# Kernel tuning notes

Hardware: AMD Instinct MI355X
Metric: run time of the kernel (lower is better)

## Reference

```python
import jax, jax.numpy as jnp
import numpy as np

NCE_T = 0.07


def setup_inputs() -> dict:
    key = jax.random.key(0)
    k1, k2, k3 = jax.random.split(key, 3)
    features_1 = jax.random.normal(k1, (1, 20000, 256), dtype=jnp.float32)
    features_2 = jax.random.normal(k2, (1, 8192, 256), dtype=jnp.float32)
    map21 = jax.random.randint(k3, (8192,), 0, 20000, dtype=jnp.int64)
    return {"features_1": features_1, "features_2": features_2, "map21": map21}


def reference(features_1, features_2, map21):
    # squeeze leading batch dim (module assumes batch size 1)
    f1 = features_1[0]  # [N1, D]
    f2 = features_2[0]  # [P, D]  (P == nce_num_pairs == len(map21) -> arange branch)
    query = f1[map21]   # [P, D] gather
    keys = f2           # [P, D]
    # pairwise Euclidean distance via matmul trick (matches torch.cdist p=2)
    q_sq = jnp.sum(query * query, axis=-1)  # [P]
    k_sq = jnp.sum(keys * keys, axis=-1)    # [P]
    sq_dist = q_sq[:, None] + k_sq[None, :] - 2.0 * (query @ keys.T)  # [P, P]
    dist = jnp.sqrt(jnp.maximum(sq_dist, 0.0))
    logits = -dist / NCE_T
    # cross entropy with labels = arange(P): mean of -log_softmax diagonal
    logp = jax.nn.log_softmax(logits, axis=-1)
    loss = -jnp.mean(jnp.diagonal(logp))
    return loss
```

## Files before the change

### kernel.cpp

```cpp
#include <hip/hip_runtime.h>
#include <hip/hip_bf16.h>

#define PP       8192
#define DIM      256
#define GS16     4096
#define NCHUNK   16
#define TCOLS    32
#define ROWBLK   256
#define NROWBLK  (PP / ROWBLK)

typedef __bf16 bf16_t;
using bf16x8 = __attribute__((ext_vector_type(8))) __bf16;
using bf16x4 = __attribute__((ext_vector_type(4))) __bf16;
using f32x4  = __attribute__((ext_vector_type(4))) float;

#define C2    20.609929155556618
#define MEXP  (-340.0f)
#define COEF  ((float)(-C2 * 8388608.0))
#define KBIAS ((float)((127.0 + 340.0) * 8388608.0))
#define LN2   0.6931471805599453f


__global__ __launch_bounds__(256) void nce_prep(
    const float* __restrict__ f1, const float* __restrict__ f2,
    const int* __restrict__ map,
    bf16_t* __restrict__ qb2, bf16_t* __restrict__ kb2,
    float* __restrict__ qsq, float* __restrict__ ksq,
    float* __restrict__ diag2, float* __restrict__ part_l,
    unsigned* __restrict__ cnt, float* __restrict__ out)
{
    const int tid  = threadIdx.x;
    const int wave = tid >> 6, lane = tid & 63;
    const int p    = blockIdx.x * 4 + wave;
    const int gtid = blockIdx.x * 256 + tid;

    if (gtid < PP) part_l[gtid] = 0.0f;
    if (gtid < NROWBLK) cnt[gtid] = 0u;
    if (gtid == 0) out[0] = 0.0f;

    const int idx = map[p];
    const f32x4 qv = *(const f32x4*)(f1 + (size_t)idx * DIM + lane * 4);
    const f32x4 kv = *(const f32x4*)(f2 + (size_t)p * DIM + lane * 4);

    float qs = qv[0]*qv[0] + qv[1]*qv[1] + qv[2]*qv[2] + qv[3]*qv[3];
    float ks = kv[0]*kv[0] + kv[1]*kv[1] + kv[2]*kv[2] + kv[3]*kv[3];
    const f32x4 dv = qv - kv;
    float ds = dv[0]*dv[0] + dv[1]*dv[1] + dv[2]*dv[2] + dv[3]*dv[3];

    bf16x4 qo, ko;
    #pragma unroll
    for (int i = 0; i < 4; ++i) { qo[i] = (bf16_t)qv[i]; ko[i] = (bf16_t)kv[i]; }

    const int G = p >> 4, l15 = p & 15;
    const size_t off = (size_t)G * GS16 + (size_t)(lane >> 3) * 512
                     + (size_t)(l15 + 16 * ((lane >> 1) & 3)) * 8 + (lane & 1) * 4;
    *(bf16x4*)(qb2 + off) = qo;
    *(bf16x4*)(kb2 + off) = ko;

    #pragma unroll
    for (int s = 32; s > 0; s >>= 1) {
        qs += __shfl_xor(qs, s);
        ks += __shfl_xor(ks, s);
        ds += __shfl_xor(ds, s);
    }
    if (lane == 0) {
        qsq[p]   = qs;
        ksq[p]   = ks;
        diag2[p] = (float)(-C2) * __builtin_amdgcn_sqrtf(ds);
    }
}

__global__ __launch_bounds__(256, 2) void nce_main(
    const bf16_t* __restrict__ qb2, const bf16_t* __restrict__ kb2,
    const float* __restrict__ qsq, const float* __restrict__ ksq,
    const float* __restrict__ diag2, float* __restrict__ part_l,
    unsigned* __restrict__ cnt, float* __restrict__ out)
{
    const int tid  = threadIdx.x, wave = tid >> 6, lane = tid & 63;
    const int quad = lane >> 4, l15 = lane & 15;
    const int rb   = blockIdx.x;
    const int ch   = blockIdx.y;
    const int Gb   = rb * 16 + wave * 4;
    const int rbase = rb * ROWBLK + wave * 64;

    __shared__ int   s_last;
    __shared__ float red[4];

    bf16x8 a[4][8];
    {
        const bf16_t* ap = qb2 + (size_t)Gb * GS16 + lane * 8;
        #pragma unroll
        for (int rg = 0; rg < 4; ++rg)
            #pragma unroll
            for (int f = 0; f < 8; ++f)
                a[rg][f] = *(const bf16x8*)(ap + rg * GS16 + f * 512);
    }

    float qs[16];
    #pragma unroll
    for (int i = 0; i < 16; ++i)
        qs[i] = qsq[rbase + (i >> 2) * 16 + quad * 4 + (i & 3)];

    float l[16];
    #pragma unroll
    for (int i = 0; i < 16; ++i) l[i] = 0.0f;

    const bf16_t* tb = kb2 + (size_t)ch * 32 * GS16 + lane * 8;
    bf16x8 br[4];
    #pragma unroll
    for (int s = 0; s < 4; ++s) br[s] = *(const bf16x8*)(tb + s * 512);
    const float* kqp = ksq + ch * 512 + l15;

    for (int t = 0; t < TCOLS; ++t) {
        const float kq = kqp[t * 16];
        f32x4 acc0 = {0,0,0,0}, acc1 = {0,0,0,0}, acc2 = {0,0,0,0}, acc3 = {0,0,0,0};
        #pragma unroll
        for (int f = 0; f < 8; ++f) {
            const bf16x8 b = br[f & 3];
            acc0 = __builtin_amdgcn_mfma_f32_16x16x32_bf16(a[0][f], b, acc0, 0, 0, 0);
            acc1 = __builtin_amdgcn_mfma_f32_16x16x32_bf16(a[1][f], b, acc1, 0, 0, 0);
            acc2 = __builtin_amdgcn_mfma_f32_16x16x32_bf16(a[2][f], b, acc2, 0, 0, 0);
            acc3 = __builtin_amdgcn_mfma_f32_16x16x32_bf16(a[3][f], b, acc3, 0, 0, 0);
            br[f & 3] = *(const bf16x8*)(tb + (size_t)(t * 8 + f + 4) * 512);
        }

        #pragma unroll
        for (int i = 0; i < 16; ++i) {
            const float av = (i < 4) ? acc0[i & 3] : (i < 8) ? acc1[i & 3]
                           : (i < 12) ? acc2[i & 3] : acc3[i & 3];
            const float sq = fmaxf(fmaf(-2.0f, av, qs[i] + kq), 0.0f);
            const float t0 = __builtin_amdgcn_sqrtf(sq);
            const float u0 = fmaxf(fmaf(t0, COEF, KBIAS), 0.0f);
            l[i] += __uint_as_float((unsigned)u0);
        }
    }

    #pragma unroll
    for (int s = 1; s < 16; s <<= 1) {
        #pragma unroll
        for (int i = 0; i < 16; ++i) l[i] += __shfl_xor(l[i], s);
    }

    if (l15 == 0) {
        #pragma unroll
        for (int i = 0; i < 16; ++i)
            atomicAdd(&part_l[rbase + (i >> 2) * 16 + quad * 4 + (i & 3)], l[i]);
    }

    __syncthreads();
    if (tid == 0) {
        __threadfence();
        s_last = (atomicAdd(&cnt[rb], 1u) == NCHUNK - 1) ? 1 : 0;
    }
    __syncthreads();
    if (s_last) {
        const int row = rb * ROWBLK + tid;
        const float lf = atomicAdd(&part_l[row], 0.0f);
        float v = MEXP + __builtin_amdgcn_logf(lf) - diag2[row];
        #pragma unroll
        for (int s = 1; s < 64; s <<= 1) v += __shfl_xor(v, s);
        if (lane == 0) red[wave] = v;
        __syncthreads();
        if (tid == 0)
            atomicAdd(out, (red[0] + red[1] + red[2] + red[3]) * (LN2 / (float)PP));
    }
}

extern "C" void kernel_launch(void* const* d_in, const int* in_sizes, int n_in,
                              void* d_out, int out_size, void* d_ws, size_t ws_size,
                              hipStream_t stream)
{
    const float* f1  = (const float*)d_in[0];
    const float* f2  = (const float*)d_in[1];
    const int*   map = (const int*)d_in[2];
    float* out = (float*)d_out;

    char* ws = (char*)d_ws;
    bf16_t*   qb2    = (bf16_t*)ws;
    bf16_t*   kb2    = qb2 + (size_t)512 * GS16;
    float*    qsq    = (float*)(ws + (2ull * 512 * GS16 + 4096) * sizeof(bf16_t));
    float*    ksq    = qsq + PP;
    float*    diag2  = ksq + PP;
    float*    part_l = diag2 + PP;
    unsigned* cnt    = (unsigned*)(part_l + PP);

    nce_prep<<<PP / 4, 256, 0, stream>>>(f1, f2, map, qb2, kb2, qsq, ksq,
                                         diag2, part_l, cnt, out);
    nce_main<<<dim3(NROWBLK, NCHUNK), 256, 0, stream>>>(qb2, kb2, qsq, ksq,
                                                        diag2, part_l, cnt, out);
}
```

Baseline: 133.7 us.

## Halve row block per wave, raise occupancy, remap grid, deepen B prefetch

Each wave now owns 32 rows instead of 64, which halves the A fragment registers. Launch bounds move to 3 blocks per SM and the number of row blocks doubles. The grid becomes 1D with a swizzled chunk index so that neighbouring blocks spread across K chunks, and the B prefetch is a full 8-fragment double buffer with split accumulators and a prefetched ksq. The aim is more parallelism and latency hiding, in exchange for half the A reuse per B load, which doubles B traffic from L2.

```diff
diff --git a/kernel.cpp b/kernel.cpp
--- a/kernel.cpp
+++ b/kernel.cpp
@@ -6,7 +6,7 @@
 #define GS16     4096
 #define NCHUNK   16
 #define TCOLS    32
-#define ROWBLK   256
+#define ROWBLK   128
 #define NROWBLK  (PP / ROWBLK)
 
 typedef __bf16 bf16_t;
@@ -70,7 +70,7 @@
     }
 }
 
-__global__ __launch_bounds__(256, 2) void nce_main(
+__global__ __launch_bounds__(256, 3) void nce_main(
     const bf16_t* __restrict__ qb2, const bf16_t* __restrict__ kb2,
     const float* __restrict__ qsq, const float* __restrict__ ksq,
     const float* __restrict__ diag2, float* __restrict__ part_l,
@@ -78,72 +78,72 @@
 {
     const int tid  = threadIdx.x, wave = tid >> 6, lane = tid & 63;
     const int quad = lane >> 4, l15 = lane & 15;
-    const int rb   = blockIdx.x;
-    const int ch   = blockIdx.y;
-    const int Gb   = rb * 16 + wave * 4;
-    const int rbase = rb * ROWBLK + wave * 64;
+    const int gid  = blockIdx.x;
+    const int ch   = (gid & 7) * 2 + ((gid >> 3) & 1);
+    const int rb   = gid >> 4;
+    const int Gb   = rb * 8 + wave * 2;
+    const int rbase = rb * ROWBLK + wave * 32;
 
     __shared__ int   s_last;
     __shared__ float red[4];
 
-    bf16x8 a[4][8];
+    bf16x8 a[2][8];
     {
         const bf16_t* ap = qb2 + (size_t)Gb * GS16 + lane * 8;
         #pragma unroll
-        for (int rg = 0; rg < 4; ++rg)
+        for (int rg = 0; rg < 2; ++rg)
             #pragma unroll
             for (int f = 0; f < 8; ++f)
                 a[rg][f] = *(const bf16x8*)(ap + rg * GS16 + f * 512);
     }
 
-    float qs[16];
+    float qs[8];
     #pragma unroll
-    for (int i = 0; i < 16; ++i)
+    for (int i = 0; i < 8; ++i)
         qs[i] = qsq[rbase + (i >> 2) * 16 + quad * 4 + (i & 3)];
 
-    float l[16];
+    float l[8];
     #pragma unroll
-    for (int i = 0; i < 16; ++i) l[i] = 0.0f;
+    for (int i = 0; i < 8; ++i) l[i] = 0.0f;
 
     const bf16_t* tb = kb2 + (size_t)ch * 32 * GS16 + lane * 8;
-    bf16x8 br[4];
+    bf16x8 br[8];
     #pragma unroll
-    for (int s = 0; s < 4; ++s) br[s] = *(const bf16x8*)(tb + s * 512);
+    for (int f = 0; f < 8; ++f) br[f] = *(const bf16x8*)(tb + f * 512);
     const float* kqp = ksq + ch * 512 + l15;
+    float kqc = kqp[0];
 
     for (int t = 0; t < TCOLS; ++t) {
-        const float kq = kqp[t * 16];
-        f32x4 acc0 = {0,0,0,0}, acc1 = {0,0,0,0}, acc2 = {0,0,0,0}, acc3 = {0,0,0,0};
+        const float kqn = kqp[(t + 1) * 16];
+        f32x4 acc[2][2] = {{{0,0,0,0},{0,0,0,0}},{{0,0,0,0},{0,0,0,0}}};
         #pragma unroll
         for (int f = 0; f < 8; ++f) {
-            const bf16x8 b = br[f & 3];
-            acc0 = __builtin_amdgcn_mfma_f32_16x16x32_bf16(a[0][f], b, acc0, 0, 0, 0);
-            acc1 = __builtin_amdgcn_mfma_f32_16x16x32_bf16(a[1][f], b, acc1, 0, 0, 0);
-            acc2 = __builtin_amdgcn_mfma_f32_16x16x32_bf16(a[2][f], b, acc2, 0, 0, 0);
-            acc3 = __builtin_amdgcn_mfma_f32_16x16x32_bf16(a[3][f], b, acc3, 0, 0, 0);
-            br[f & 3] = *(const bf16x8*)(tb + (size_t)(t * 8 + f + 4) * 512);
+            const bf16x8 b = br[f];
+            acc[0][f & 1] = __builtin_amdgcn_mfma_f32_16x16x32_bf16(a[0][f], b, acc[0][f & 1], 0, 0, 0);
+            acc[1][f & 1] = __builtin_amdgcn_mfma_f32_16x16x32_bf16(a[1][f], b, acc[1][f & 1], 0, 0, 0);
+            br[f] = *(const bf16x8*)(tb + (size_t)((t + 1) * 8 + f) * 512);
         }
 
         #pragma unroll
-        for (int i = 0; i < 16; ++i) {
-            const float av = (i < 4) ? acc0[i & 3] : (i < 8) ? acc1[i & 3]
-                           : (i < 12) ? acc2[i & 3] : acc3[i & 3];
-            const float sq = fmaxf(fmaf(-2.0f, av, qs[i] + kq), 0.0f);
+        for (int i = 0; i < 8; ++i) {
+            const float av = acc[i >> 2][0][i & 3] + acc[i >> 2][1][i & 3];
+            const float sq = fmaxf(fmaf(-2.0f, av, qs[i] + kqc), 0.0f);
             const float t0 = __builtin_amdgcn_sqrtf(sq);
             const float u0 = fmaxf(fmaf(t0, COEF, KBIAS), 0.0f);
             l[i] += __uint_as_float((unsigned)u0);
         }
+        kqc = kqn;
     }
 
     #pragma unroll
     for (int s = 1; s < 16; s <<= 1) {
         #pragma unroll
-        for (int i = 0; i < 16; ++i) l[i] += __shfl_xor(l[i], s);
+        for (int i = 0; i < 8; ++i) l[i] += __shfl_xor(l[i], s);
     }
 
     if (l15 == 0) {
         #pragma unroll
-        for (int i = 0; i < 16; ++i)
+        for (int i = 0; i < 8; ++i)
             atomicAdd(&part_l[rbase + (i >> 2) * 16 + quad * 4 + (i & 3)], l[i]);
     }
 
@@ -154,9 +154,12 @@
     }
     __syncthreads();
     if (s_last) {
-        const int row = rb * ROWBLK + tid;
-        const float lf = atomicAdd(&part_l[row], 0.0f);
-        float v = MEXP + __builtin_amdgcn_logf(lf) - diag2[row];
+        float v = 0.0f;
+        if (tid < ROWBLK) {
+            const int row = rb * ROWBLK + tid;
+            const float lf = atomicAdd(&part_l[row], 0.0f);
+            v = MEXP + __builtin_amdgcn_logf(lf) - diag2[row];
+        }
         #pragma unroll
         for (int s = 1; s < 64; s <<= 1) v += __shfl_xor(v, s);
         if (lane == 0) red[wave] = v;
@@ -186,6 +189,6 @@
 
     nce_prep<<<PP / 4, 256, 0, stream>>>(f1, f2, map, qb2, kb2, qsq, ksq,
                                          diag2, part_l, cnt, out);
-    nce_main<<<dim3(NROWBLK, NCHUNK), 256, 0, stream>>>(qb2, kb2, qsq, ksq,
-                                                        diag2, part_l, cnt, out);
+    nce_main<<<NROWBLK * NCHUNK, 256, 0, stream>>>(qb2, kb2, qsq, ksq,
+                                                   diag2, part_l, cnt, out);
 }
```

New measurement: 134.8 us. No clear change (+0.9%).
